# Performance work log

Hardware: AMD Instinct MI355X
Metric: run time of the kernel (lower is better)

The kernel has to match this reference:

```python
import jax, jax.numpy as jnp
import numpy as np

B, H, P, K, E, BN = 8, 256, 1024, 32, 4, 64


def setup_inputs() -> dict:
    key = jax.random.key(0)
    ks = jax.random.split(key, 8)
    current = jax.random.normal(ks[0], (B, H, P), dtype=jnp.float32)
    neighbor_features = jax.random.normal(ks[1], (B, H, P, K), dtype=jnp.float32)
    # binary {0,1} validity mask, stored as float like the torch module expects
    neighbor_validity = jax.random.randint(ks[2], (B, 1, P, K), 0, 2).astype(jnp.float32)
    edge_features = jax.random.normal(ks[3], (B, E, P, K), dtype=jnp.float32)
    # 1x1 Conv2d weights flattened to matrices: (out_ch, in_ch)
    w1 = jax.random.normal(ks[4], (BN, 2 * H + E), dtype=jnp.float32) * 0.05
    b1 = jnp.zeros((BN,), dtype=jnp.float32)
    w2 = jax.random.normal(ks[5], (BN,), dtype=jnp.float32) * 0.05  # second conv: out_ch=1
    b2 = jnp.zeros((), dtype=jnp.float32)
    return {
        "current": current,
        "neighbor_features": neighbor_features,
        "neighbor_validity": neighbor_validity,
        "edge_features": edge_features,
        "w1": w1,
        "b1": b1,
        "w2": w2,
        "b2": b2,
    }


def reference(current, neighbor_features, neighbor_validity, edge_features, w1, b1, w2, b2):
    h_dim = current.shape[1]
    # Split the 1x1-conv weight along the concat axis so we never materialize
    # the [B, 2H+E, P, K] concatenated tensor (same math as cat + conv1x1).
    w1c = w1[:, :h_dim]            # acts on broadcast center features
    w1n = w1[:, h_dim:2 * h_dim]   # acts on neighbor features
    w1e = w1[:, 2 * h_dim:]        # acts on edge features

    hid = (
        jnp.einsum("bcp,oc->bop", current, w1c)[:, :, :, None]
        + jnp.einsum("bcpk,oc->bopk", neighbor_features, w1n)
        + jnp.einsum("bcpk,oc->bopk", edge_features, w1e)
        + b1[None, :, None, None]
    )
    hid = jax.nn.relu(hid)                                  # (B, BN, P, K)
    logits = jnp.einsum("bopk,o->bpk", hid, w2) + b2        # (B, P, K)

    valid = neighbor_validity[:, 0] > 0.5                   # (B, P, K) bool
    logits = jnp.where(valid, logits, -jnp.inf)
    has_any = jnp.any(valid, axis=-1, keepdims=True)        # (B, P, 1)
    logits_safe = jnp.where(has_any, logits, 0.0)           # all-masked rows -> 0 logits
    weights = jax.nn.softmax(logits_safe, axis=-1)
    weights = jnp.where(has_any & valid, weights, 0.0)      # zero weight on pads / empty rows

    pooled = jnp.einsum("bcpk,bpk->bcp", neighbor_features, weights)
    return pooled
```

## Files before the change

kernel.cpp:

```cpp
#include <hip/hip_runtime.h>
#include <math.h>


#define B_ 8
#define H_ 256
#define P_ 1024
#define K_ 32
#define E_ 4
#define BN_ 64

typedef __attribute__((ext_vector_type(8))) short short8;
typedef __attribute__((ext_vector_type(4))) float floatx4;

__device__ __forceinline__ unsigned short bf16_rne(float f) {
  unsigned u = __float_as_uint(f);
  u += 0x7fffu + ((u >> 16) & 1u);
  return (unsigned short)(u >> 16);
}
__device__ __forceinline__ unsigned pack_bf16_rne(float lo, float hi) {
  unsigned u0 = __float_as_uint(lo);
  u0 += 0x7fffu + ((u0 >> 16) & 1u);
  unsigned u1 = __float_as_uint(hi);
  u1 += 0x7fffu + ((u1 >> 16) & 1u);
  return (u0 >> 16) | (u1 & 0xffff0000u);
}
__device__ __forceinline__ float bf16_to_f(unsigned short u) {
  return __uint_as_float(((unsigned)u) << 16);
}

__global__ __launch_bounds__(256) void prep_kernel(
    const float* __restrict__ w1, unsigned short* __restrict__ w1m) {
  int i = blockIdx.x * 256 + threadIdx.x;
  if (i >= 4 * 17 * 64 * 8) return;
  int j = i & 7, lane = (i >> 3) & 63;
  int kt = i >> 9;
  int tm = kt / 17, ki = kt % 17;
  int o = tm * 16 + (lane & 15);
  int c = ki * 32 + (lane >> 4) * 8 + j;
  float v = (c < 516) ? w1[o * 516 + c] : 0.f;
  w1m[i] = bf16_rne(v);
}

__global__ __launch_bounds__(256, 4) void soft_attn_agg_kernel(
    const float* __restrict__ cur,
    const float* __restrict__ nf,
    const float* __restrict__ nv,
    const float* __restrict__ ef,
    const unsigned short* __restrict__ w1m,
    const float* __restrict__ b1,
    const float* __restrict__ w2,
    float* __restrict__ out) {
  constexpr int NFROW = 264;
  __shared__ unsigned short s_nfT[K_][NFROW];
  __shared__ unsigned short s_curb[H_];
  __shared__ unsigned short s_edgeT[K_][4];
  __shared__ float s_valid[K_];
  __shared__ float s_b1[BN_];
  __shared__ float s_w2[BN_];
  __shared__ float s_lg[4][2][16];
  __shared__ float s_wt[K_];

  const int t = threadIdx.x;
  const unsigned bid = blockIdx.x;
  const unsigned xcd = bid & 7u, sidx = bid >> 3;
  const int p = (int)(xcd * 128u + (sidx & 127u));
  const int b = (int)(sidx >> 7);

  const int w = t >> 6;
  const int lane = t & 63;
  const int q = lane >> 4;
  const int ln15 = lane & 15;

  const float* nf_base = nf + ((size_t)b * H_ * P_ + (size_t)p) * K_;
  {
    const int kk = lane & 31, ch = lane >> 5;
#pragma unroll
    for (int oc8 = 0; oc8 < 8; ++oc8) {
      const int c = (w * 8 + oc8) * 8 + ch * 4;
      const float* gp = nf_base + (size_t)c * (P_ * K_) + kk;
      float f0 = gp[0];
      float f1 = gp[(size_t)P_ * K_];
      float f2 = gp[(size_t)(2 * P_) * K_];
      float f3 = gp[(size_t)(3 * P_) * K_];
      uint2 d;
      d.x = pack_bf16_rne(f0, f1);
      d.y = pack_bf16_rne(f2, f3);
      *(uint2*)&s_nfT[kk][c] = d;
    }
  }
  s_curb[t] = bf16_rne(cur[((size_t)b * H_ + t) * P_ + p]);
  if (t < K_) {
    const float* ep = ef + ((size_t)b * E_ * P_ + (size_t)p) * K_ + t;
    float e0 = ep[0];
    float e1 = ep[(size_t)P_ * K_];
    float e2 = ep[(size_t)(2 * P_) * K_];
    float e3 = ep[(size_t)(3 * P_) * K_];
    uint2 d;
    d.x = pack_bf16_rne(e0, e1);
    d.y = pack_bf16_rne(e2, e3);
    *(uint2*)&s_edgeT[t][0] = d;
  } else if (t < 64) {
    s_valid[t - 32] = nv[((size_t)b * P_ + p) * K_ + (t - 32)];
  } else if (t < 128) {
    s_b1[t - 64] = b1[t - 64];
  } else if (t < 192) {
    s_w2[t - 128] = w2[t - 128];
  }
  __syncthreads();

  floatx4 acc0, acc1;
  {
    const int ob = w * 16 + q * 4;
    float b0v = s_b1[ob + 0], b1v = s_b1[ob + 1];
    float b2v = s_b1[ob + 2], b3v = s_b1[ob + 3];
    acc0[0] = b0v; acc0[1] = b1v; acc0[2] = b2v; acc0[3] = b3v;
    acc1[0] = b0v; acc1[1] = b1v; acc1[2] = b2v; acc1[3] = b3v;
  }
  const unsigned short* w1m_w = w1m + ((size_t)(w * 17) * 64 + lane) * 8;

#pragma unroll
  for (int ki = 0; ki < 8; ++ki) {
    short8 a = *(const short8*)(w1m_w + (size_t)ki * 512);
    short8 bb = *(const short8*)&s_curb[ki * 32 + q * 8];
    acc0 = __builtin_amdgcn_mfma_f32_16x16x32_bf16(a, bb, acc0, 0, 0, 0);
    acc1 = __builtin_amdgcn_mfma_f32_16x16x32_bf16(a, bb, acc1, 0, 0, 0);
  }
#pragma unroll
  for (int ki = 0; ki < 8; ++ki) {
    short8 a = *(const short8*)(w1m_w + (size_t)(8 + ki) * 512);
    const int c0 = ki * 32 + q * 8;
    short8 b0 = *(const short8*)&s_nfT[ln15][c0];
    short8 b1f = *(const short8*)&s_nfT[16 + ln15][c0];
    acc0 = __builtin_amdgcn_mfma_f32_16x16x32_bf16(a, b0, acc0, 0, 0, 0);
    acc1 = __builtin_amdgcn_mfma_f32_16x16x32_bf16(a, b1f, acc1, 0, 0, 0);
  }
  {
    short8 a = *(const short8*)(w1m_w + (size_t)16 * 512);
    uint2 e0 = *(const uint2*)&s_edgeT[ln15][0];
    uint2 e1 = *(const uint2*)&s_edgeT[16 + ln15][0];
    union { unsigned u[4]; short8 s; } ub0, ub1;
    ub0.u[0] = (q == 0) ? e0.x : 0u;
    ub0.u[1] = (q == 0) ? e0.y : 0u;
    ub0.u[2] = 0u; ub0.u[3] = 0u;
    ub1.u[0] = (q == 0) ? e1.x : 0u;
    ub1.u[1] = (q == 0) ? e1.y : 0u;
    ub1.u[2] = 0u; ub1.u[3] = 0u;
    acc0 = __builtin_amdgcn_mfma_f32_16x16x32_bf16(a, ub0.s, acc0, 0, 0, 0);
    acc1 = __builtin_amdgcn_mfma_f32_16x16x32_bf16(a, ub1.s, acc1, 0, 0, 0);
  }

  {
    float lp0 = 0.f, lp1 = 0.f;
#pragma unroll
    for (int r = 0; r < 4; ++r) {
      float w2o = s_w2[w * 16 + q * 4 + r];
      lp0 = fmaf(fmaxf(acc0[r], 0.f), w2o, lp0);
      lp1 = fmaf(fmaxf(acc1[r], 0.f), w2o, lp1);
    }
    lp0 += __shfl_xor(lp0, 16);
    lp0 += __shfl_xor(lp0, 32);
    lp1 += __shfl_xor(lp1, 16);
    lp1 += __shfl_xor(lp1, 32);
    if (lane < 16) {
      s_lg[w][0][lane] = lp0;
      s_lg[w][1][lane] = lp1;
    }
  }
  __syncthreads();

  if (t < K_) {
    const int tn = t >> 4, col = t & 15;
    float lg = s_lg[0][tn][col] + s_lg[1][tn][col] + s_lg[2][tn][col] +
               s_lg[3][tn][col];
    bool v = s_valid[t] > 0.5f;
    float ml = v ? lg : -INFINITY;
#pragma unroll
    for (int m = 1; m < 32; m <<= 1) ml = fmaxf(ml, __shfl_xor(ml, m));
    float e = v ? __expf(lg - ml) : 0.f;
    float ssum = e;
#pragma unroll
    for (int m = 1; m < 32; m <<= 1) ssum += __shfl_xor(ssum, m);
    s_wt[t] = (ml > -INFINITY) ? (e / ssum) : 0.f;
  }
  __syncthreads();

  {
    float accp = 0.f;
#pragma unroll
    for (int kk = 0; kk < K_; kk += 2) {
      float2 wt2 = *(const float2*)&s_wt[kk];
      float f0 = bf16_to_f(s_nfT[kk][t]);
      float f1 = bf16_to_f(s_nfT[kk + 1][t]);
      accp = fmaf(f1, wt2.y, fmaf(f0, wt2.x, accp));
    }
    out[((size_t)b * H_ + t) * P_ + p] = accp;
  }
}

extern "C" void kernel_launch(void* const* d_in, const int* in_sizes, int n_in,
                              void* d_out, int out_size, void* d_ws,
                              size_t ws_size, hipStream_t stream) {
  const float* cur = (const float*)d_in[0];
  const float* nf  = (const float*)d_in[1];
  const float* nv  = (const float*)d_in[2];
  const float* ef  = (const float*)d_in[3];
  const float* w1  = (const float*)d_in[4];
  const float* b1  = (const float*)d_in[5];
  const float* w2  = (const float*)d_in[6];

  unsigned short* w1m = (unsigned short*)d_ws;
  prep_kernel<<<(4 * 17 * 64 * 8 + 255) / 256, 256, 0, stream>>>(w1, w1m);
  soft_attn_agg_kernel<<<B_ * P_, 256, 0, stream>>>(
      cur, nf, nv, ef, w1m, b1, w2, (float*)d_out);
}
```

Before: 405.9 us.

## Process two points per block with float4 loads and swizzled LDS layout

Each block now handles two adjacent points (64 neighbor columns) instead of one, halving the grid. Each wave computes all four output-row tiles for its own 16 neighbor columns, reusing one B fragment across four MFMAs. Neighbor features are loaded with float4 (four consecutive k per lane), which is more coalesced than the prior scalar loads, and stored as channel-pair dwords with an XOR swizzle to avoid LDS bank conflicts. The cost is more LDS per block, which may lower occupancy, and more w1m fragment loads per wave.

```diff
diff --git a/kernel.cpp b/kernel.cpp
--- a/kernel.cpp
+++ b/kernel.cpp
@@ -24,9 +24,6 @@
   u1 += 0x7fffu + ((u1 >> 16) & 1u);
   return (u0 >> 16) | (u1 & 0xffff0000u);
 }
-__device__ __forceinline__ float bf16_to_f(unsigned short u) {
-  return __uint_as_float(((unsigned)u) << 16);
-}
 
 __global__ __launch_bounds__(256) void prep_kernel(
     const float* __restrict__ w1, unsigned short* __restrict__ w1m) {
@@ -34,8 +31,8 @@
   if (i >= 4 * 17 * 64 * 8) return;
   int j = i & 7, lane = (i >> 3) & 63;
   int kt = i >> 9;
-  int tm = kt / 17, ki = kt % 17;
-  int o = tm * 16 + (lane & 15);
+  int mt = kt / 17, ki = kt % 17;
+  int o = mt * 16 + (lane & 15);
   int c = ki * 32 + (lane >> 4) * 8 + j;
   float v = (c < 516) ? w1[o * 516 + c] : 0.f;
   w1m[i] = bf16_rne(v);
@@ -50,57 +47,62 @@
     const float* __restrict__ b1,
     const float* __restrict__ w2,
     float* __restrict__ out) {
-  constexpr int NFROW = 264;
-  __shared__ unsigned short s_nfT[K_][NFROW];
-  __shared__ unsigned short s_curb[H_];
-  __shared__ unsigned short s_edgeT[K_][4];
-  __shared__ float s_valid[K_];
-  __shared__ float s_b1[BN_];
-  __shared__ float s_w2[BN_];
-  __shared__ float s_lg[4][2][16];
-  __shared__ float s_wt[K_];
+  __shared__ unsigned s_nf_dw[BN_ * 132];
+  __shared__ __align__(16) unsigned short s_curb[2][H_];
+  __shared__ __align__(16) unsigned short s_edgeT[2][K_][8];
+  __shared__ float s_valid[64];
+  __shared__ __align__(16) float s_b1[BN_];
+  __shared__ __align__(16) float s_w2[BN_];
+  __shared__ float s_lg[BN_];
+  __shared__ float s_wt[64];
 
   const int t = threadIdx.x;
   const unsigned bid = blockIdx.x;
   const unsigned xcd = bid & 7u, sidx = bid >> 3;
-  const int p = (int)(xcd * 128u + (sidx & 127u));
-  const int b = (int)(sidx >> 7);
+  const int p0 = (int)(2u * (xcd * 64u + (sidx & 63u)));
+  const int b = (int)(sidx >> 6);
 
   const int w = t >> 6;
   const int lane = t & 63;
   const int q = lane >> 4;
   const int ln15 = lane & 15;
 
-  const float* nf_base = nf + ((size_t)b * H_ * P_ + (size_t)p) * K_;
-  {
-    const int kk = lane & 31, ch = lane >> 5;
-#pragma unroll
-    for (int oc8 = 0; oc8 < 8; ++oc8) {
-      const int c = (w * 8 + oc8) * 8 + ch * 4;
-      const float* gp = nf_base + (size_t)c * (P_ * K_) + kk;
-      float f0 = gp[0];
-      float f1 = gp[(size_t)P_ * K_];
-      float f2 = gp[(size_t)(2 * P_) * K_];
-      float f3 = gp[(size_t)(3 * P_) * K_];
-      uint2 d;
-      d.x = pack_bf16_rne(f0, f1);
-      d.y = pack_bf16_rne(f2, f3);
-      *(uint2*)&s_nfT[kk][c] = d;
-    }
-  }
-  s_curb[t] = bf16_rne(cur[((size_t)b * H_ + t) * P_ + p]);
-  if (t < K_) {
-    const float* ep = ef + ((size_t)b * E_ * P_ + (size_t)p) * K_ + t;
+  {
+    const int r = lane >> 4, s = lane & 15;
+    const float* base = nf + ((size_t)b * H_ * P_ + (size_t)p0) * K_;
+    const int X = (s & 14) << 1;
+    unsigned* dst0 = s_nf_dw + (4 * s) * 132;
+#pragma unroll
+    for (int i = 0; i < 8; ++i) {
+      const int c_even = w * 64 + i * 8 + 2 * r;
+      const float4 fa = *(const float4*)(base + (size_t)c_even * (P_ * K_) + s * 4);
+      const float4 fb = *(const float4*)(base + (size_t)(c_even + 1) * (P_ * K_) + s * 4);
+      const int cp = (32 * w + 4 * i + r) ^ X;
+      unsigned* dst = dst0 + cp;
+      dst[0]   = pack_bf16_rne(fa.x, fb.x);
+      dst[132] = pack_bf16_rne(fa.y, fb.y);
+      dst[264] = pack_bf16_rne(fa.z, fb.z);
+      dst[396] = pack_bf16_rne(fa.w, fb.w);
+    }
+  }
+  {
+    const float* cp_ = cur + ((size_t)b * H_ + t) * P_ + p0;
+    s_curb[0][t] = bf16_rne(cp_[0]);
+    s_curb[1][t] = bf16_rne(cp_[1]);
+  }
+  if (t < 64) {
+    s_valid[t] = nv[((size_t)b * P_ + p0) * K_ + t];
+    const int pl = t >> 5, k = t & 31;
+    const float* ep = ef + (((size_t)b * E_ * P_) + p0 + pl) * K_ + k;
     float e0 = ep[0];
     float e1 = ep[(size_t)P_ * K_];
     float e2 = ep[(size_t)(2 * P_) * K_];
     float e3 = ep[(size_t)(3 * P_) * K_];
-    uint2 d;
+    uint4 d;
     d.x = pack_bf16_rne(e0, e1);
     d.y = pack_bf16_rne(e2, e3);
-    *(uint2*)&s_edgeT[t][0] = d;
-  } else if (t < 64) {
-    s_valid[t - 32] = nv[((size_t)b * P_ + p) * K_ + (t - 32)];
+    d.z = 0u; d.w = 0u;
+    *(uint4*)&s_edgeT[pl][k][0] = d;
   } else if (t < 128) {
     s_b1[t - 64] = b1[t - 64];
   } else if (t < 192) {
@@ -108,70 +110,51 @@
   }
   __syncthreads();
 
-  floatx4 acc0, acc1;
-  {
-    const int ob = w * 16 + q * 4;
-    float b0v = s_b1[ob + 0], b1v = s_b1[ob + 1];
-    float b2v = s_b1[ob + 2], b3v = s_b1[ob + 3];
-    acc0[0] = b0v; acc0[1] = b1v; acc0[2] = b2v; acc0[3] = b3v;
-    acc1[0] = b0v; acc1[1] = b1v; acc1[2] = b2v; acc1[3] = b3v;
-  }
-  const unsigned short* w1m_w = w1m + ((size_t)(w * 17) * 64 + lane) * 8;
-
-#pragma unroll
-  for (int ki = 0; ki < 8; ++ki) {
-    short8 a = *(const short8*)(w1m_w + (size_t)ki * 512);
-    short8 bb = *(const short8*)&s_curb[ki * 32 + q * 8];
-    acc0 = __builtin_amdgcn_mfma_f32_16x16x32_bf16(a, bb, acc0, 0, 0, 0);
-    acc1 = __builtin_amdgcn_mfma_f32_16x16x32_bf16(a, bb, acc1, 0, 0, 0);
-  }
-#pragma unroll
-  for (int ki = 0; ki < 8; ++ki) {
-    short8 a = *(const short8*)(w1m_w + (size_t)(8 + ki) * 512);
-    const int c0 = ki * 32 + q * 8;
-    short8 b0 = *(const short8*)&s_nfT[ln15][c0];
-    short8 b1f = *(const short8*)&s_nfT[16 + ln15][c0];
-    acc0 = __builtin_amdgcn_mfma_f32_16x16x32_bf16(a, b0, acc0, 0, 0, 0);
-    acc1 = __builtin_amdgcn_mfma_f32_16x16x32_bf16(a, b1f, acc1, 0, 0, 0);
-  }
-  {
-    short8 a = *(const short8*)(w1m_w + (size_t)16 * 512);
-    uint2 e0 = *(const uint2*)&s_edgeT[ln15][0];
-    uint2 e1 = *(const uint2*)&s_edgeT[16 + ln15][0];
-    union { unsigned u[4]; short8 s; } ub0, ub1;
-    ub0.u[0] = (q == 0) ? e0.x : 0u;
-    ub0.u[1] = (q == 0) ? e0.y : 0u;
-    ub0.u[2] = 0u; ub0.u[3] = 0u;
-    ub1.u[0] = (q == 0) ? e1.x : 0u;
-    ub1.u[1] = (q == 0) ? e1.y : 0u;
-    ub1.u[2] = 0u; ub1.u[3] = 0u;
-    acc0 = __builtin_amdgcn_mfma_f32_16x16x32_bf16(a, ub0.s, acc0, 0, 0, 0);
-    acc1 = __builtin_amdgcn_mfma_f32_16x16x32_bf16(a, ub1.s, acc1, 0, 0, 0);
-  }
-
-  {
-    float lp0 = 0.f, lp1 = 0.f;
-#pragma unroll
-    for (int r = 0; r < 4; ++r) {
-      float w2o = s_w2[w * 16 + q * 4 + r];
-      lp0 = fmaf(fmaxf(acc0[r], 0.f), w2o, lp0);
-      lp1 = fmaf(fmaxf(acc1[r], 0.f), w2o, lp1);
-    }
-    lp0 += __shfl_xor(lp0, 16);
-    lp0 += __shfl_xor(lp0, 32);
-    lp1 += __shfl_xor(lp1, 16);
-    lp1 += __shfl_xor(lp1, 32);
-    if (lane < 16) {
-      s_lg[w][0][lane] = lp0;
-      s_lg[w][1][lane] = lp1;
-    }
+  floatx4 acc[4];
+#pragma unroll
+  for (int mt = 0; mt < 4; ++mt)
+    acc[mt] = *(const floatx4*)&s_b1[mt * 16 + q * 4];
+
+  const int pl_w = w >> 1;
+  const int n_lane = 16 * w + ln15;
+  const int bxor = ((2 * w + (ln15 >> 3)) & 7) << 2;
+  const unsigned* bsrc = s_nf_dw + n_lane * 132;
+  const unsigned short* w1m_l = w1m + (size_t)lane * 8;
+
+#pragma unroll
+  for (int ki = 0; ki < 17; ++ki) {
+    short8 bfrag;
+    if (ki < 8) {
+      bfrag = *(const short8*)&s_curb[pl_w][ki * 32 + q * 8];
+    } else if (ki < 16) {
+      bfrag = *(const short8*)(bsrc + ((16 * (ki - 8) + 4 * q) ^ bxor));
+    } else {
+      bfrag = *(const short8*)&s_edgeT[pl_w][(w & 1) * 16 + ln15][0];
+    }
+#pragma unroll
+    for (int mt = 0; mt < 4; ++mt) {
+      short8 a = *(const short8*)(w1m_l + (size_t)(mt * 17 + ki) * 512);
+      acc[mt] = __builtin_amdgcn_mfma_f32_16x16x32_bf16(a, bfrag, acc[mt], 0, 0, 0);
+    }
+  }
+
+  {
+    float lp = 0.f;
+#pragma unroll
+    for (int mt = 0; mt < 4; ++mt) {
+      const floatx4 w2v = *(const floatx4*)&s_w2[mt * 16 + q * 4];
+#pragma unroll
+      for (int r = 0; r < 4; ++r)
+        lp = fmaf(fmaxf(acc[mt][r], 0.f), w2v[r], lp);
+    }
+    lp += __shfl_xor(lp, 16);
+    lp += __shfl_xor(lp, 32);
+    if (lane < 16) s_lg[16 * w + lane] = lp;
   }
   __syncthreads();
 
-  if (t < K_) {
-    const int tn = t >> 4, col = t & 15;
-    float lg = s_lg[0][tn][col] + s_lg[1][tn][col] + s_lg[2][tn][col] +
-               s_lg[3][tn][col];
+  if (t < 64) {
+    float lg = s_lg[t];
     bool v = s_valid[t] > 0.5f;
     float ml = v ? lg : -INFINITY;
 #pragma unroll
@@ -185,15 +168,20 @@
   __syncthreads();
 
   {
-    float accp = 0.f;
-#pragma unroll
-    for (int kk = 0; kk < K_; kk += 2) {
-      float2 wt2 = *(const float2*)&s_wt[kk];
-      float f0 = bf16_to_f(s_nfT[kk][t]);
-      float f1 = bf16_to_f(s_nfT[kk + 1][t]);
-      accp = fmaf(f1, wt2.y, fmaf(f0, wt2.x, accp));
-    }
-    out[((size_t)b * H_ + t) * P_ + p] = accp;
+    const int pl = t >> 7, cpair = t & 127;
+    float acc0 = 0.f, acc1 = 0.f;
+#pragma unroll
+    for (int k = 0; k < K_; ++k) {
+      const int n = pl * 32 + k;
+      const int xr = ((n >> 3) & 7) << 2;
+      const unsigned u = s_nf_dw[n * 132 + (cpair ^ xr)];
+      const float wtk = s_wt[n];
+      acc0 = fmaf(__uint_as_float(u << 16), wtk, acc0);
+      acc1 = fmaf(__uint_as_float(u & 0xffff0000u), wtk, acc1);
+    }
+    float* op = out + ((size_t)b * H_ + 2 * cpair) * P_ + p0 + pl;
+    op[0] = acc0;
+    op[P_] = acc1;
   }
 }
 
@@ -210,6 +198,6 @@
 
   unsigned short* w1m = (unsigned short*)d_ws;
   prep_kernel<<<(4 * 17 * 64 * 8 + 255) / 256, 256, 0, stream>>>(w1, w1m);
-  soft_attn_agg_kernel<<<B_ * P_, 256, 0, stream>>>(
+  soft_attn_agg_kernel<<<B_ * P_ / 2, 256, 0, stream>>>(
       cur, nf, nv, ef, w1m, b1, w2, (float*)d_out);
 }
```

Measured after the change: 417.5 us. 1.03x slower.
